# Kernel tuning notes

Measured on AMD Instinct MI355X. Metric: run time of the kernel, lower is better.

Reference implementation:

```python
import jax, jax.numpy as jnp
import numpy as np

# Hardcoded Mamba2 config from the torch module: d_model=32, d_state=8, d_conv=2,
# expand=2, headdim=8 -> d_inner=64, nheads=8, ngroups=1.
IN_DIM = 36
D_MODEL = 32
D_INNER = 64
D_STATE = 8
NHEADS = 8
HEADDIM = 8
D_CONV = 2
CONV_DIM = D_INNER + 2 * D_STATE            # 80
D_IN_PROJ = 2 * D_INNER + 2 * D_STATE + NHEADS  # 152
NORM_EPS = 1e-5


def setup_inputs() -> dict:
    key = jax.random.key(0)
    ks = jax.random.split(key, 12)
    N = 524288
    x = jax.random.normal(ks[0], (N, IN_DIM), dtype=jnp.float32)
    # f_out: Linear(36 -> 32)
    f_out_w = jax.random.normal(ks[1], (D_MODEL, IN_DIM), jnp.float32) / np.sqrt(IN_DIM)
    f_out_b = jax.random.normal(ks[2], (D_MODEL,), jnp.float32) * 0.02
    # Mamba2 params
    in_proj_w = jax.random.normal(ks[3], (D_IN_PROJ, D_MODEL), jnp.float32) / np.sqrt(D_MODEL)
    conv_w = jax.random.normal(ks[4], (CONV_DIM, D_CONV), jnp.float32) / np.sqrt(D_CONV)  # depthwise taps
    conv_b = jax.random.normal(ks[5], (CONV_DIM,), jnp.float32) * 0.02
    dt_bias = jnp.log(jnp.exp(jax.random.uniform(ks[6], (NHEADS,), jnp.float32,
                                                 minval=1e-3, maxval=0.1)) - 1.0)  # inv softplus of dt init
    A_log = jnp.log(jax.random.uniform(ks[7], (NHEADS,), jnp.float32, minval=1.0, maxval=16.0))
    D_skip = jnp.ones((NHEADS,), jnp.float32) + 0.02 * jax.random.normal(ks[8], (NHEADS,), jnp.float32)
    norm_w = jnp.ones((D_INNER,), jnp.float32) + 0.02 * jax.random.normal(ks[9], (D_INNER,), jnp.float32)
    out_proj_w = jax.random.normal(ks[10], (D_MODEL, D_INNER), jnp.float32) / np.sqrt(D_INNER)
    return {"x": x, "f_out_w": f_out_w, "f_out_b": f_out_b, "in_proj_w": in_proj_w,
            "conv_w": conv_w, "conv_b": conv_b, "dt_bias": dt_bias, "A_log": A_log,
            "D_skip": D_skip, "norm_w": norm_w, "out_proj_w": out_proj_w}


def reference(x, f_out_w, f_out_b, in_proj_w, conv_w, conv_b, dt_bias, A_log,
              D_skip, norm_w, out_proj_w):
    N = x.shape[0]
    # f_out: (N,36) -> (N,32); seq_len is 1 so we keep everything 2-D.
    u = x @ f_out_w.T + f_out_b
    # in_proj -> split [z | xBC | dt]
    zxbcdt = u @ in_proj_w.T                                  # (N,152)
    z = zxbcdt[:, :D_INNER]                                   # (N,64)
    xBC = zxbcdt[:, D_INNER:D_INNER + CONV_DIM]               # (N,80)
    dt = zxbcdt[:, D_INNER + CONV_DIM:]                       # (N,8)
    # causal depthwise conv over seq (len 1, kernel 2): only the last tap sees data
    xBC = jax.nn.silu(xBC * conv_w[:, -1] + conv_b)
    xh = xBC[:, :D_INNER].reshape(N, NHEADS, HEADDIM)         # (N,8,8)
    Bm = xBC[:, D_INNER:D_INNER + D_STATE]                    # (N,8)
    Cm = xBC[:, D_INNER + D_STATE:]                           # (N,8)
    dt = jax.nn.softplus(dt + dt_bias)                        # (N,8)
    # Selective scan with seq_len=1 and h0=0: h = dt * B (x) x ; y = C.h + D*x.
    # exp(dt * (-exp(A_log))) multiplies the zero initial state, so A_log drops out.
    bc = jnp.sum(Bm * Cm, axis=-1)                            # (N,)
    y = xh * (dt * bc[:, None])[:, :, None] + D_skip[None, :, None] * xh
    y = y.reshape(N, D_INNER)
    # RMSNormGated (gate first, then norm; single group)
    y = y * jax.nn.silu(z)
    y = y * jax.lax.rsqrt(jnp.mean(y * y, axis=-1, keepdims=True) + NORM_EPS) * norm_w
    out = y @ out_proj_w.T                                    # (N,32)
    return jax.nn.softmax(out, axis=1)
```

## Files before the change

### kernel.cpp

```cpp
#include <hip/hip_runtime.h>
#include <math.h>

typedef _Float16 half8 __attribute__((ext_vector_type(8)));
typedef _Float16 half4 __attribute__((ext_vector_type(4)));
typedef float floatx4 __attribute__((ext_vector_type(4)));

constexpr int IN_DIM = 36;
constexpr int BLOCKS = 1024;

__device__ __forceinline__ float fast_rcp(float v) { return __builtin_amdgcn_rcpf(v); }
__device__ __forceinline__ float silu_f(float v) { return v * fast_rcp(1.0f + __expf(-v)); }
__device__ __forceinline__ float softplus_f(float v) {
    return fmaxf(v, 0.0f) + __logf(1.0f + __expf(-fabsf(v)));
}

extern "C" __global__ void __launch_bounds__(64)
prep_kernel(const float* __restrict__ f_out_w, const float* __restrict__ f_out_b,
            const float* __restrict__ in_proj_w, const float* __restrict__ conv_w,
            const float* __restrict__ conv_b, const float* __restrict__ dt_bias,
            const float* __restrict__ norm_w, const float* __restrict__ out_proj_w,
            void* __restrict__ ws) {
    const int fid = blockIdx.x;
    const int L = threadIdx.x;
    const int c = L & 15, q = L >> 4;
    unsigned short* fr = (unsigned short*)ws;
    for (int j = 0; j < 8; ++j) {
        float val = 0.f;
        if (fid < 20) {
            const int t = fid >> 1, ks = fid & 1;
            const int m = t * 16 + c;
            const int k = ks * 32 + q * 8 + j;
            if (m < 152) {
                if (k < IN_DIM) {
                    float acc = 0.f;
                    for (int mm = 0; mm < 32; ++mm)
                        acc += f_out_w[mm * IN_DIM + k] * in_proj_w[m * 32 + mm];
                    if (m >= 64 && m < 144) acc *= conv_w[(m - 64) * 2 + 1];
                    val = acc;
                } else if (k == IN_DIM) {
                    float acc = 0.f;
                    for (int mm = 0; mm < 32; ++mm)
                        acc += f_out_b[mm] * in_proj_w[m * 32 + mm];
                    if (m >= 64 && m < 144)      val = acc * conv_w[(m - 64) * 2 + 1] + conv_b[m - 64];
                    else if (m >= 144)           val = acc + dt_bias[m - 144];
                    else                         val = acc;
                }
            }
        } else {
            const int mt = (fid - 20) >> 1, ks = (fid - 20) & 1;
            const int m = mt * 16 + c;
            const int k = ks * 32 + q * 8 + j;
            val = out_proj_w[m * 64 + k] * norm_w[k];
        }
        _Float16 h = (_Float16)val;
        fr[fid * 512 + L * 8 + j] = __builtin_bit_cast(unsigned short, h);
    }
}

extern "C" __global__ void __launch_bounds__(256, 3)
mamba_mfma_kernel(const float* __restrict__ x,
                  const float* __restrict__ D_skip,
                  const void* __restrict__ ws,
                  float* __restrict__ out,
                  int tiles_per_wave) {
    __shared__ _Float16 ldsY[4][16 * 72];
    const int lane = threadIdx.x & 63;
    const int wv   = threadIdx.x >> 6;
    const int c = lane & 15, q = lane >> 4;

    const char* wsb = (const char*)ws;
    half8 A2[10][2], A3[2][2];
#pragma unroll
    for (int t = 0; t < 10; ++t)
#pragma unroll
        for (int ks = 0; ks < 2; ++ks)
            A2[t][ks] = *(const half8*)(wsb + (size_t)((t * 2 + ks) * 64 + lane) * 16);
#pragma unroll
    for (int mt = 0; mt < 2; ++mt)
#pragma unroll
        for (int ks = 0; ks < 2; ++ks)
            A3[mt][ks] = *(const half8*)(wsb + (size_t)((20 + mt * 2 + ks) * 64 + lane) * 16);

    const float4 dskv = *(const float4*)(D_skip + (q & 1) * 4);
    _Float16* myL = ldsY[wv];

    const long rowBase = (long)(blockIdx.x * 4 + wv) * tiles_per_wave * 16;
    const float* xrow = x + (rowBase + c) * (long)IN_DIM;

    float4 xa, xb, xct;
    {
        const float* p = xrow + q * 8;
        xa = *(const float4*)p;
        xb = *(const float4*)(p + 4);
        xct = (q == 0) ? *(const float4*)(xrow + 32) : make_float4(0.f, 0.f, 0.f, 0.f);
    }

#pragma unroll 1
    for (int tile = 0; tile < tiles_per_wave; ++tile) {
        float4 na = xa, nb = xb, nc2 = xct;
        if (tile + 1 < tiles_per_wave) {
            const float* p = xrow + (size_t)(tile + 1) * 16 * IN_DIM + q * 8;
            na = *(const float4*)p;
            nb = *(const float4*)(p + 4);
            if (q == 0) nc2 = *(const float4*)(xrow + (size_t)(tile + 1) * 16 * IN_DIM + 32);
        }

        const _Float16 zh = (_Float16)0.f;
        half8 Bx0, Bx1;
        Bx0[0] = (_Float16)xa.x; Bx0[1] = (_Float16)xa.y;
        Bx0[2] = (_Float16)xa.z; Bx0[3] = (_Float16)xa.w;
        Bx0[4] = (_Float16)xb.x; Bx0[5] = (_Float16)xb.y;
        Bx0[6] = (_Float16)xb.z; Bx0[7] = (_Float16)xb.w;
        Bx1[0] = (q == 0) ? (_Float16)xct.x : zh;
        Bx1[1] = (q == 0) ? (_Float16)xct.y : zh;
        Bx1[2] = (q == 0) ? (_Float16)xct.z : zh;
        Bx1[3] = (q == 0) ? (_Float16)xct.w : zh;
        Bx1[4] = (q == 0) ? (_Float16)1.0f : zh;
        Bx1[5] = zh; Bx1[6] = zh; Bx1[7] = zh;

        floatx4 acc[10];
#pragma unroll
        for (int t = 0; t < 10; ++t) {
            floatx4 z4 = {0.f, 0.f, 0.f, 0.f};
            z4 = __builtin_amdgcn_mfma_f32_16x16x32_f16(A2[t][0], Bx0, z4, 0, 0, 0);
            acc[t] = __builtin_amdgcn_mfma_f32_16x16x32_f16(A2[t][1], Bx1, z4, 0, 0, 0);
        }

#pragma unroll
        for (int t = 4; t <= 8; ++t)
#pragma unroll
            for (int r = 0; r < 4; ++r) acc[t][r] = silu_f(acc[t][r]);

        float recv[4];
#pragma unroll
        for (int r = 0; r < 4; ++r) recv[r] = __shfl_xor(acc[8][r], 32, 64);
        float part = 0.f;
#pragma unroll
        for (int r = 0; r < 4; ++r) part = __builtin_fmaf(acc[8][r], recv[r], part);
        const float bc = part + __shfl_xor(part, 16, 64);

        float scale[4];
#pragma unroll
        for (int r = 0; r < 4; ++r)
            scale[r] = __builtin_fmaf(softplus_f(acc[9][r]), bc, dskv[r]);
        float s0[4], s1[4];
#pragma unroll
        for (int r = 0; r < 4; ++r) {
            s0[r] = __shfl(scale[r], c, 64);
            s1[r] = __shfl(scale[r], c + 16, 64);
        }
        const bool hb = (q >= 2);
        float sclA[4];
        sclA[0] = hb ? s0[1] : s0[0];
        sclA[1] = hb ? s0[3] : s0[2];
        sclA[2] = hb ? s1[1] : s1[0];
        sclA[3] = hb ? s1[3] : s1[2];

        float yv[4][4];
        float ssum = 0.f;
#pragma unroll
        for (int t = 0; t < 4; ++t)
#pragma unroll
            for (int r = 0; r < 4; ++r) {
                float v = acc[4 + t][r] * sclA[t] * silu_f(acc[t][r]);
                yv[t][r] = v;
                ssum = __builtin_fmaf(v, v, ssum);
            }
        ssum += __shfl_xor(ssum, 16, 64);
        ssum += __shfl_xor(ssum, 32, 64);
        const float rs = __builtin_amdgcn_rsqf(__builtin_fmaf(ssum, 1.0f / 64.0f, 1e-5f));

#pragma unroll
        for (int t = 0; t < 4; ++t) {
            half4 h = {(_Float16)yv[t][0], (_Float16)yv[t][1],
                       (_Float16)yv[t][2], (_Float16)yv[t][3]};
            *(half4*)(myL + c * 72 + 16 * t + 4 * q) = h;
        }
        half8 By0 = *(const half8*)(myL + c * 72 + 8 * q);
        half8 By1 = *(const half8*)(myL + c * 72 + 32 + 8 * q);

        floatx4 z4 = {0.f, 0.f, 0.f, 0.f};
        floatx4 lg0 = __builtin_amdgcn_mfma_f32_16x16x32_f16(A3[0][0], By0, z4, 0, 0, 0);
        lg0 = __builtin_amdgcn_mfma_f32_16x16x32_f16(A3[0][1], By1, lg0, 0, 0, 0);
        floatx4 lg1 = __builtin_amdgcn_mfma_f32_16x16x32_f16(A3[1][0], By0, z4, 0, 0, 0);
        lg1 = __builtin_amdgcn_mfma_f32_16x16x32_f16(A3[1][1], By1, lg1, 0, 0, 0);

        float e0[4], e1[4];
        float lsum = 0.f;
#pragma unroll
        for (int r = 0; r < 4; ++r) {
            e0[r] = __expf(lg0[r] * rs);
            e1[r] = __expf(lg1[r] * rs);
            lsum += e0[r] + e1[r];
        }
        lsum += __shfl_xor(lsum, 16, 64);
        lsum += __shfl_xor(lsum, 32, 64);
        const float inv = fast_rcp(lsum);

        const long orow = rowBase + (long)tile * 16 + c;
        *(float4*)(out + orow * 32 + 4 * q) =
            make_float4(e0[0] * inv, e0[1] * inv, e0[2] * inv, e0[3] * inv);
        *(float4*)(out + orow * 32 + 16 + 4 * q) =
            make_float4(e1[0] * inv, e1[1] * inv, e1[2] * inv, e1[3] * inv);

        xa = na; xb = nb; xct = nc2;
    }
}

extern "C" void kernel_launch(void* const* d_in, const int* in_sizes, int n_in,
                              void* d_out, int out_size, void* d_ws, size_t ws_size,
                              hipStream_t stream) {
    const float* x          = (const float*)d_in[0];
    const float* f_out_w    = (const float*)d_in[1];
    const float* f_out_b    = (const float*)d_in[2];
    const float* in_proj_w  = (const float*)d_in[3];
    const float* conv_w     = (const float*)d_in[4];
    const float* conv_b     = (const float*)d_in[5];
    const float* dt_bias    = (const float*)d_in[6];
    const float* D_skip     = (const float*)d_in[8];
    const float* norm_w     = (const float*)d_in[9];
    const float* out_proj_w = (const float*)d_in[10];
    float* out = (float*)d_out;

    const int n = in_sizes[0] / IN_DIM;
    const int tiles_per_wave = n / (BLOCKS * 4 * 16);

    hipLaunchKernelGGL(prep_kernel, dim3(24), dim3(64), 0, stream,
                       f_out_w, f_out_b, in_proj_w, conv_w, conv_b, dt_bias,
                       norm_w, out_proj_w, d_ws);
    hipLaunchKernelGGL(mamba_mfma_kernel, dim3(BLOCKS), dim3(256), 0, stream,
                       x, D_skip, d_ws, out, tiles_per_wave);
}
```

Before: 163.8 us.

## Pack fp16 conversions, merge silu reciprocals, use exp2, raise occupancy

Replaces per-element fp16 conversions with packed cvt_pkrtz for the MFMA B operand and the LDS store. Combines the two silu reciprocals in the gating product into one reciprocal of the product of denominators. Switches the softmax exponential to native exp2 with a prescaled factor. Doubles the grid to 2048 blocks and raises the launch bound minimum to 5 blocks per CU, which limits registers per thread and risks spills. The xct value is no longer masked for q!=0 lanes; it is zero there anyway, and the product of denominators can overflow for large negative inputs.

```diff
diff --git a/kernel.cpp b/kernel.cpp
--- a/kernel.cpp
+++ b/kernel.cpp
@@ -3,15 +3,20 @@
 
 typedef _Float16 half8 __attribute__((ext_vector_type(8)));
 typedef _Float16 half4 __attribute__((ext_vector_type(4)));
+typedef __fp16 fp16x2 __attribute__((ext_vector_type(2)));
 typedef float floatx4 __attribute__((ext_vector_type(4)));
 
 constexpr int IN_DIM = 36;
-constexpr int BLOCKS = 1024;
+constexpr int BLOCKS = 2048;
 
 __device__ __forceinline__ float fast_rcp(float v) { return __builtin_amdgcn_rcpf(v); }
 __device__ __forceinline__ float silu_f(float v) { return v * fast_rcp(1.0f + __expf(-v)); }
 __device__ __forceinline__ float softplus_f(float v) {
     return fmaxf(v, 0.0f) + __logf(1.0f + __expf(-fabsf(v)));
+}
+__device__ __forceinline__ float pk2f(float a, float b) {
+    fp16x2 p = __builtin_amdgcn_cvt_pkrtz(a, b);
+    return __builtin_bit_cast(float, p);
 }
 
 extern "C" __global__ void __launch_bounds__(64)
@@ -57,7 +62,7 @@
     }
 }
 
-extern "C" __global__ void __launch_bounds__(256, 3)
+extern "C" __global__ void __launch_bounds__(256, 5)
 mamba_mfma_kernel(const float* __restrict__ x,
                   const float* __restrict__ D_skip,
                   const void* __restrict__ ws,
@@ -105,31 +110,26 @@
             if (q == 0) nc2 = *(const float4*)(xrow + (size_t)(tile + 1) * 16 * IN_DIM + 32);
         }
 
-        const _Float16 zh = (_Float16)0.f;
-        half8 Bx0, Bx1;
-        Bx0[0] = (_Float16)xa.x; Bx0[1] = (_Float16)xa.y;
-        Bx0[2] = (_Float16)xa.z; Bx0[3] = (_Float16)xa.w;
-        Bx0[4] = (_Float16)xb.x; Bx0[5] = (_Float16)xb.y;
-        Bx0[6] = (_Float16)xb.z; Bx0[7] = (_Float16)xb.w;
-        Bx1[0] = (q == 0) ? (_Float16)xct.x : zh;
-        Bx1[1] = (q == 0) ? (_Float16)xct.y : zh;
-        Bx1[2] = (q == 0) ? (_Float16)xct.z : zh;
-        Bx1[3] = (q == 0) ? (_Float16)xct.w : zh;
-        Bx1[4] = (q == 0) ? (_Float16)1.0f : zh;
-        Bx1[5] = zh; Bx1[6] = zh; Bx1[7] = zh;
+        union { half8 h; float4 f; } bx0, bx1;
+        bx0.f.x = pk2f(xa.x, xa.y);
+        bx0.f.y = pk2f(xa.z, xa.w);
+        bx0.f.z = pk2f(xb.x, xb.y);
+        bx0.f.w = pk2f(xb.z, xb.w);
+        bx1.f.x = pk2f(xct.x, xct.y);
+        bx1.f.y = pk2f(xct.z, xct.w);
+        bx1.f.z = (q == 0) ? pk2f(1.0f, 0.0f) : 0.0f;
+        bx1.f.w = 0.0f;
 
         floatx4 acc[10];
 #pragma unroll
         for (int t = 0; t < 10; ++t) {
             floatx4 z4 = {0.f, 0.f, 0.f, 0.f};
-            z4 = __builtin_amdgcn_mfma_f32_16x16x32_f16(A2[t][0], Bx0, z4, 0, 0, 0);
-            acc[t] = __builtin_amdgcn_mfma_f32_16x16x32_f16(A2[t][1], Bx1, z4, 0, 0, 0);
-        }
-
-#pragma unroll
-        for (int t = 4; t <= 8; ++t)
-#pragma unroll
-            for (int r = 0; r < 4; ++r) acc[t][r] = silu_f(acc[t][r]);
+            z4 = __builtin_amdgcn_mfma_f32_16x16x32_f16(A2[t][0], bx0.h, z4, 0, 0, 0);
+            acc[t] = __builtin_amdgcn_mfma_f32_16x16x32_f16(A2[t][1], bx1.h, z4, 0, 0, 0);
+        }
+
+#pragma unroll
+        for (int r = 0; r < 4; ++r) acc[8][r] = silu_f(acc[8][r]);
 
         float recv[4];
 #pragma unroll
@@ -162,7 +162,9 @@
         for (int t = 0; t < 4; ++t)
 #pragma unroll
             for (int r = 0; r < 4; ++r) {
-                float v = acc[4 + t][r] * sclA[t] * silu_f(acc[t][r]);
+                const float zr = acc[t][r], xh = acc[4 + t][r];
+                const float den = (1.0f + __expf(-zr)) * (1.0f + __expf(-xh));
+                const float v = zr * xh * sclA[t] * fast_rcp(den);
                 yv[t][r] = v;
                 ssum = __builtin_fmaf(v, v, ssum);
             }
@@ -172,9 +174,10 @@
 
 #pragma unroll
         for (int t = 0; t < 4; ++t) {
-            half4 h = {(_Float16)yv[t][0], (_Float16)yv[t][1],
-                       (_Float16)yv[t][2], (_Float16)yv[t][3]};
-            *(half4*)(myL + c * 72 + 16 * t + 4 * q) = h;
+            union { half4 h; float2 f; } w;
+            w.f.x = pk2f(yv[t][0], yv[t][1]);
+            w.f.y = pk2f(yv[t][2], yv[t][3]);
+            *(half4*)(myL + c * 72 + 16 * t + 4 * q) = w.h;
         }
         half8 By0 = *(const half8*)(myL + c * 72 + 8 * q);
         half8 By1 = *(const half8*)(myL + c * 72 + 32 + 8 * q);
@@ -185,12 +188,13 @@
         floatx4 lg1 = __builtin_amdgcn_mfma_f32_16x16x32_f16(A3[1][0], By0, z4, 0, 0, 0);
         lg1 = __builtin_amdgcn_mfma_f32_16x16x32_f16(A3[1][1], By1, lg1, 0, 0, 0);
 
+        const float rs2 = rs * 1.44269504f;
         float e0[4], e1[4];
         float lsum = 0.f;
 #pragma unroll
         for (int r = 0; r < 4; ++r) {
-            e0[r] = __expf(lg0[r] * rs);
-            e1[r] = __expf(lg1[r] * rs);
+            e0[r] = __builtin_amdgcn_exp2f(lg0[r] * rs2);
+            e1[r] = __builtin_amdgcn_exp2f(lg1[r] * rs2);
             lsum += e0[r] + e1[r];
         }
         lsum += __shfl_xor(lsum, 16, 64);
```

Measured after the change: 285.3 us. 1.74x slower.
